# Optimization experiments

Measured on AMD Instinct MI355X. Metric: run time of the kernel, lower is better.

The kernel has to match this reference:

```python
import jax, jax.numpy as jnp
import numpy as np

N = 2048   # total nodes (16 graphs x 128 EEG channels)
BS = 16    # number of graphs
E = 65536  # directed edges
LENIN = 8500
H = 640


def _lstm_layer(x, w_ih, w_hh, b_ih, b_hh):
    # x: [T, in]; torch gate order i, f, g, o. Input projection hoisted out of scan.
    hdim = w_hh.shape[1]
    xp = x @ w_ih.T + (b_ih + b_hh)  # [T, 4H]
    def step(carry, xt):
        h, c = carry
        g = xt + h @ w_hh.T
        i, f, gg, o = jnp.split(g, 4)
        c = jax.nn.sigmoid(f) * c + jax.nn.sigmoid(i) * jnp.tanh(gg)
        h = jax.nn.sigmoid(o) * jnp.tanh(c)
        return (h, c), h
    init = (jnp.zeros((hdim,), x.dtype), jnp.zeros((hdim,), x.dtype))
    _, hs = jax.lax.scan(step, init, xp)
    return hs  # [T, H]


def _gcn(x, W, b, src, dst, n):
    # PyG GCNConv: add self-loops, symmetric deg^-1/2 normalization, scatter-add at target.
    xw = x @ W
    loop = jnp.arange(n)
    s = jnp.concatenate([src, loop])
    d = jnp.concatenate([dst, loop])
    deg = jax.ops.segment_sum(jnp.ones(d.shape[0], xw.dtype), d, num_segments=n)
    dinv = jnp.where(deg > 0, jax.lax.rsqrt(jnp.maximum(deg, 1e-12)), 0.0)
    norm = dinv[s] * dinv[d]
    out = jax.ops.segment_sum(xw[s] * norm[:, None], d, num_segments=n)
    return out + b


def _bn(x):
    # F.batch_norm(training=True, no running stats, no affine): biased var, eps=1e-5
    mu = jnp.mean(x, axis=0)
    var = jnp.mean((x - mu) ** 2, axis=0)
    return (x - mu) * jax.lax.rsqrt(var + 1e-5)


def _lrelu(x):
    return jnp.where(x >= 0, x, 0.01 * x)


def setup_inputs() -> dict:
    key = jax.random.key(0)
    ks = jax.random.split(key, 32)
    s = 0.05
    inp = {}
    inp['x_in'] = jax.random.normal(ks[0], (N, LENIN), dtype=jnp.float32)
    inp['edge_index'] = jax.random.randint(ks[1], (2, E), 0, N).astype(jnp.int64)
    # LSTM: 3 layers
    ins = [LENIN, H, H]
    for l in range(3):
        inp[f'lstm_w_ih_{l}'] = s * jax.random.normal(ks[2 + 4 * l], (4 * H, ins[l]), dtype=jnp.float32)
        inp[f'lstm_w_hh_{l}'] = s * jax.random.normal(ks[3 + 4 * l], (4 * H, H), dtype=jnp.float32)
        inp[f'lstm_b_ih_{l}'] = s * jax.random.normal(ks[4 + 4 * l], (4 * H,), dtype=jnp.float32)
        inp[f'lstm_b_hh_{l}'] = s * jax.random.normal(ks[5 + 4 * l], (4 * H,), dtype=jnp.float32)
    # GCN layers
    dims = [(640, 320), (320, 180), (180, 90), (90, 50)]
    for i, (di, do) in enumerate(dims, 1):
        inp[f'gcn_w{i}'] = s * jax.random.normal(ks[14 + 2 * i], (di, do), dtype=jnp.float32)
        inp[f'gcn_b{i}'] = jnp.zeros((do,), dtype=jnp.float32)
    # FC head
    fdims = [(50, 32), (32, 16), (16, 1)]
    for i, (di, do) in enumerate(fdims, 1):
        inp[f'fc_w{i}'] = s * jax.random.normal(ks[24 + 2 * i], (di, do), dtype=jnp.float32)
        inp[f'fc_b{i}'] = jnp.zeros((do,), dtype=jnp.float32)
    return inp


def reference(x_in, edge_index,
              lstm_w_ih_0, lstm_w_hh_0, lstm_b_ih_0, lstm_b_hh_0,
              lstm_w_ih_1, lstm_w_hh_1, lstm_b_ih_1, lstm_b_hh_1,
              lstm_w_ih_2, lstm_w_hh_2, lstm_b_ih_2, lstm_b_hh_2,
              gcn_w1, gcn_b1, gcn_w2, gcn_b2, gcn_w3, gcn_b3, gcn_w4, gcn_b4,
              fc_w1, fc_b1, fc_w2, fc_b2, fc_w3, fc_b3):
    x = _lstm_layer(x_in, lstm_w_ih_0, lstm_w_hh_0, lstm_b_ih_0, lstm_b_hh_0)
    x = _lstm_layer(x, lstm_w_ih_1, lstm_w_hh_1, lstm_b_ih_1, lstm_b_hh_1)
    x = _lstm_layer(x, lstm_w_ih_2, lstm_w_hh_2, lstm_b_ih_2, lstm_b_hh_2)
    src, dst = edge_index[0], edge_index[1]
    x = _bn(_lrelu(_gcn(x, gcn_w1, gcn_b1, src, dst, N)))
    x = _bn(_lrelu(_gcn(x, gcn_w2, gcn_b2, src, dst, N)))
    x = _bn(_lrelu(_gcn(x, gcn_w3, gcn_b3, src, dst, N)))
    x = _bn(_lrelu(_gcn(x, gcn_w4, gcn_b4, src, dst, N)))
    # global_add_pool with batch = i // (N // BS): contiguous blocks -> reshape-sum
    emb = x.reshape(BS, N // BS, -1).sum(axis=1)  # [BS, 50]
    y = ((emb @ fc_w1 + fc_b1) @ fc_w2 + fc_b2) @ fc_w3 + fc_b3  # [BS, 1]
    return y, emb
```

## Files before the change

### kernel.cpp

```cpp
#include <hip/hip_runtime.h>
#include <stdint.h>

#define NNODES 2048
#define T_SEQ  2048
#define HD     640
#define GD     2560
#define KIN    8500
#define NEDGE  65536
#define NGRAPH 16
#define SB     64
#define SDP    10
#define REC64  256

typedef unsigned long long u64;
typedef _Float16 half2v __attribute__((ext_vector_type(2)));
using short8 = __attribute__((ext_vector_type(8))) short;
using f32x4  = __attribute__((ext_vector_type(4))) float;

#if __has_builtin(__builtin_amdgcn_fdot2)
#define HAVE_FDOT2 1
#endif

__device__ __forceinline__ float dot2acc(unsigned w, unsigned h, float acc) {
#ifdef HAVE_FDOT2
  return __builtin_amdgcn_fdot2(__builtin_bit_cast(half2v, w),
                                __builtin_bit_cast(half2v, h), acc, false);
#else
  acc += (float)__builtin_bit_cast(_Float16, (unsigned short)(w & 0xffffu)) *
         (float)__builtin_bit_cast(_Float16, (unsigned short)(h & 0xffffu));
  acc += (float)__builtin_bit_cast(_Float16, (unsigned short)(w >> 16)) *
         (float)__builtin_bit_cast(_Float16, (unsigned short)(h >> 16));
  return acc;
#endif
}

__device__ __forceinline__ unsigned short f2h(float x) {
  return __builtin_bit_cast(unsigned short, (_Float16)x);
}
__device__ __forceinline__ unsigned packh(float a, float b) {
  return (unsigned)f2h(a) | ((unsigned)f2h(b) << 16);
}
__device__ __forceinline__ unsigned f2bf(float x) {
  unsigned u = __float_as_uint(x);
  return (u + 0x7fffu + ((u >> 16) & 1u)) >> 16;
}
__device__ __forceinline__ unsigned packbf(float a, float b) {
  return f2bf(a) | (f2bf(b) << 16);
}

#define GK 32
__global__ __launch_bounds__(256) void gemm_mfma(
    const float* __restrict__ A, const float* __restrict__ W,
    const float* __restrict__ b1, const float* __restrict__ b2,
    float* __restrict__ C, int M, int N, int K) {
  __shared__ __align__(16) short As[128 * 40];
  __shared__ __align__(16) short Ws[128 * 40];
  const int tid = threadIdx.x;
  const int wave = tid >> 6, lane = tid & 63;
  const int bm = blockIdx.y * 128, bn = blockIdx.x * 128;
  const int wm = (wave >> 1) * 64, wn = (wave & 1) * 64;
  const int mrow = lane & 15, quad = lane >> 4;
  const int srow = tid >> 1, skc = (tid & 1) * 16;
  f32x4 acc[4][4] = {};
  for (int k0 = 0; k0 < K; k0 += GK) {
    float av[16], wv[16];
    if (k0 + GK <= K) {
      const float* Ap = A + (long)(bm + srow) * K + k0 + skc;
      const float* Wp = W + (long)(bn + srow) * K + k0 + skc;
#pragma unroll
      for (int i = 0; i < 4; i++) {
        float4 a4 = *(const float4*)(Ap + 4 * i);
        float4 w4 = *(const float4*)(Wp + 4 * i);
        av[4*i]=a4.x; av[4*i+1]=a4.y; av[4*i+2]=a4.z; av[4*i+3]=a4.w;
        wv[4*i]=w4.x; wv[4*i+1]=w4.y; wv[4*i+2]=w4.z; wv[4*i+3]=w4.w;
      }
    } else {
#pragma unroll
      for (int i = 0; i < 16; i++) {
        const int k = k0 + skc + i;
        av[i] = (k < K) ? A[(long)(bm + srow) * K + k] : 0.f;
        wv[i] = (k < K) ? W[(long)(bn + srow) * K + k] : 0.f;
      }
    }
    __syncthreads();
    {
      uint4* pa = (uint4*)&As[srow * 40 + skc];
      uint4* pw = (uint4*)&Ws[srow * 40 + skc];
      pa[0] = make_uint4(packbf(av[0],av[1]), packbf(av[2],av[3]),
                         packbf(av[4],av[5]), packbf(av[6],av[7]));
      pa[1] = make_uint4(packbf(av[8],av[9]), packbf(av[10],av[11]),
                         packbf(av[12],av[13]), packbf(av[14],av[15]));
      pw[0] = make_uint4(packbf(wv[0],wv[1]), packbf(wv[2],wv[3]),
                         packbf(wv[4],wv[5]), packbf(wv[6],wv[7]));
      pw[1] = make_uint4(packbf(wv[8],wv[9]), packbf(wv[10],wv[11]),
                         packbf(wv[12],wv[13]), packbf(wv[14],wv[15]));
    }
    __syncthreads();
    short8 af[4], bf[4];
#pragma unroll
    for (int mi = 0; mi < 4; mi++)
      af[mi] = *(const short8*)&As[(wm + mi * 16 + mrow) * 40 + quad * 8];
#pragma unroll
    for (int ni = 0; ni < 4; ni++)
      bf[ni] = *(const short8*)&Ws[(wn + ni * 16 + mrow) * 40 + quad * 8];
#pragma unroll
    for (int mi = 0; mi < 4; mi++)
#pragma unroll
      for (int ni = 0; ni < 4; ni++)
        acc[mi][ni] = __builtin_amdgcn_mfma_f32_16x16x32_bf16(
            af[mi], bf[ni], acc[mi][ni], 0, 0, 0);
  }
#pragma unroll
  for (int ni = 0; ni < 4; ni++) {
    const int c = bn + wn + ni * 16 + mrow;
    const float bias = b1[c] + b2[c];
#pragma unroll
    for (int mi = 0; mi < 4; mi++) {
      const int r0 = bm + wm + mi * 16 + quad * 4;
#pragma unroll
      for (int reg = 0; reg < 4; reg++)
        C[(long)(r0 + reg) * N + c] = acc[mi][ni][reg] + bias;
    }
  }
}

__global__ __launch_bounds__(256, 1) void fused_scan(
    const float* __restrict__ xp,
    const float* __restrict__ whh0,
    const float* __restrict__ wih1, const float* __restrict__ whh1,
    const float* __restrict__ bih1, const float* __restrict__ bhh1,
    const float* __restrict__ wih2, const float* __restrict__ whh2,
    const float* __restrict__ bih2, const float* __restrict__ bhh2,
    u64* __restrict__ rec0, u64* __restrict__ rec1, u64* __restrict__ rec2,
    float* __restrict__ hs2) {
  __shared__ uint4 wh[2 * 3200];
  __shared__ __align__(16) unsigned short hbufh[640];
  __shared__ __align__(16) unsigned short xbufh[640];
  __shared__ float pdot[2][4][40];
  const int tid = threadIdx.x;
  const int l = blockIdx.x / SB, b = blockIdx.x % SB;
  const int lane = tid & 63, wv = tid >> 6;

  const float* Wih = (l == 1) ? wih1 : wih2;
  const float* Whh = (l == 0) ? whh0 : ((l == 1) ? whh1 : whh2);
  const u64* recI = (l == 1) ? rec0 : rec1;
  u64* recO = (l == 0) ? rec0 : ((l == 1) ? rec1 : rec2);

  const int nstage = (l > 0) ? 6400 : 3200;
  for (int idx = tid; idx < nstage; idx += 256) {
    int rem = idx;
    const int mat = (rem < 3200) ? 1 : 0;
    if (mat == 0) rem -= 3200;
    const int r = rem / 80, kg = rem - r * 80;
    const int g = r / SDP, d = r - g * SDP;
    const long grow = (long)(g * HD + b * SDP + d) * HD;
    const float* wr = ((mat == 1) ? Whh : Wih) + grow + kg * 8;
    const float4 wa = *(const float4*)(wr);
    const float4 wb = *(const float4*)(wr + 4);
    wh[mat * 3200 + kg * 40 + r] =
        make_uint4(packh(wa.x, wa.y), packh(wa.z, wa.w),
                   packh(wb.x, wb.y), packh(wb.z, wb.w));
  }

  float ext = 0.f;
  int gxi = 0;
  if (wv == 0 && lane < 40) {
    const int g = lane / SDP, d = lane - g * SDP;
    gxi = g * HD + b * SDP + d;
    if (l == 0) {
      ext = xp[gxi];
    } else {
      const float* bi = (l == 1) ? bih1 : bih2;
      const float* bh = (l == 1) ? bhh1 : bhh2;
      ext = bi[gxi] + bh[gxi];
    }
  }
  __syncthreads();

  const int rid = wv * 16 + (lane >> 2), j = lane & 3;
  const int ubase = rid * SDP + 3 * j;
  unsigned short* hslot = hbufh + ubase;
  unsigned short* xslot = xbufh + ubase;

  float creg = 0.f;
  for (int t = 0; t < T_SEQ; t++) {
    unsigned pend = ((t > 0) ? 1u : 0u) | ((l > 0) ? 2u : 0u);
    const long io = (long)(t - 1) * REC64 + wv * 64 + lane;
    const long iu = (long)t * REC64 + wv * 64 + lane;
    long spins = 0;
    u64 vo = 0, vu = 0;
    while (__any(pend != 0)) {
      if (pend & 1u) vo = __hip_atomic_load(recO + io, __ATOMIC_RELAXED,
                                            __HIP_MEMORY_SCOPE_AGENT);
      if (pend & 2u) vu = __hip_atomic_load(recI + iu, __ATOMIC_RELAXED,
                                            __HIP_MEMORY_SCOPE_AGENT);
      if ((pend & 1u) && (unsigned)(vo >> 48) == (unsigned)t) {
        pend &= ~1u;
        const unsigned lo = (unsigned)vo, hi = (unsigned)(vo >> 32);
        hslot[0] = (unsigned short)lo;
        if (j < 3) { hslot[1] = (unsigned short)(lo >> 16);
                     hslot[2] = (unsigned short)hi; }
      }
      if ((pend & 2u) && (unsigned)(vu >> 48) == (unsigned)(t + 1)) {
        pend &= ~2u;
        const unsigned lo = (unsigned)vu, hi = (unsigned)(vu >> 32);
        xslot[0] = (unsigned short)lo;
        if (j < 3) { xslot[1] = (unsigned short)(lo >> 16);
                     xslot[2] = (unsigned short)hi; }
      }
      if (__any(pend != 0)) {
        if (++spins > 30000000L) break;
        __builtin_amdgcn_s_sleep(1);
      }
    }
    if (t == 0) {
      hslot[0] = 0;
      if (j < 3) { hslot[1] = 0; hslot[2] = 0; }
    }
    __threadfence_block();

    if (lane < 40) {
      const int kg0 = wv * 20;
      float acc0 = 0.f, acc1 = 0.f;
      const uint4* wp = &wh[3200 + kg0 * 40 + lane];
      const uint4* hb = ((const uint4*)hbufh) + kg0;
#pragma unroll
      for (int g = 0; g < 20; g += 2) {
        const uint4 wA = wp[g * 40];
        const uint4 hA = hb[g];
        acc0 = dot2acc(wA.x, hA.x, acc0); acc0 = dot2acc(wA.y, hA.y, acc0);
        acc0 = dot2acc(wA.z, hA.z, acc0); acc0 = dot2acc(wA.w, hA.w, acc0);
        const uint4 wB = wp[(g + 1) * 40];
        const uint4 hB = hb[g + 1];
        acc1 = dot2acc(wB.x, hB.x, acc1); acc1 = dot2acc(wB.y, hB.y, acc1);
        acc1 = dot2acc(wB.z, hB.z, acc1); acc1 = dot2acc(wB.w, hB.w, acc1);
      }
      if (l > 0) {
        const uint4* wq = &wh[kg0 * 40 + lane];
        const uint4* xb = ((const uint4*)xbufh) + kg0;
#pragma unroll
        for (int g = 0; g < 20; g += 2) {
          const uint4 wA = wq[g * 40];
          const uint4 xA = xb[g];
          acc0 = dot2acc(wA.x, xA.x, acc0); acc0 = dot2acc(wA.y, xA.y, acc0);
          acc0 = dot2acc(wA.z, xA.z, acc0); acc0 = dot2acc(wA.w, xA.w, acc0);
          const uint4 wB = wq[(g + 1) * 40];
          const uint4 xB = xb[g + 1];
          acc1 = dot2acc(wB.x, xB.x, acc1); acc1 = dot2acc(wB.y, xB.y, acc1);
          acc1 = dot2acc(wB.z, xB.z, acc1); acc1 = dot2acc(wB.w, xB.w, acc1);
        }
      }
      pdot[t & 1][wv][lane] = acc0 + acc1;
    }
    __syncthreads();

    if (wv == 0) {
      const int par = t & 1;
      float av = 0.f;
      if (lane < 40) {
        const float gsum = pdot[par][0][lane] + pdot[par][1][lane] +
                           pdot[par][2][lane] + pdot[par][3][lane] + ext;
        if (lane / SDP == 2) {
          const float e2 = __expf(2.f * gsum);
          av = 1.f - 2.f / (e2 + 1.f);
        } else {
          av = 1.f / (1.f + __expf(-gsum));
        }
      }
      const float ai = av;
      const float af = __shfl(av, lane + SDP);
      const float ag = __shfl(av, lane + 2 * SDP);
      const float ao = __shfl(av, lane + 3 * SDP);
      float h = 0.f;
      if (lane < SDP) {
        creg = af * creg + ai * ag;
        const float e2 = __expf(2.f * creg);
        h = ao * (1.f - 2.f / (e2 + 1.f));
        if (l == 2) hs2[(long)t * HD + b * SDP + lane] = h;
      }
      if (l == 0 && lane < 40 && t + 1 < T_SEQ)
        ext = xp[(long)(t + 1) * GD + gxi];
      const float ha = __shfl(h, 3 * lane);
      const float hb2 = __shfl(h, 3 * lane + 1);
      const float hc = __shfl(h, 3 * lane + 2);
      if (lane < 4) {
        const unsigned seq = (unsigned)(t + 1);
        const unsigned sa = f2h(ha);
        const unsigned sb = (lane < 3) ? f2h(hb2) : 0u;
        const unsigned sc = (lane < 3) ? f2h(hc) : 0u;
        const u64 val = (u64)(sa | (sb << 16)) | ((u64)(sc | (seq << 16)) << 32);
        __hip_atomic_store(recO + (long)t * REC64 + b * 4 + lane, val,
                           __ATOMIC_RELAXED, __HIP_MEMORY_SCOPE_AGENT);
      }
    }
  }
}

__global__ __launch_bounds__(256) void gcn_gemm(
    const float* __restrict__ X, const float* __restrict__ W,
    float* __restrict__ Y, int di, int dout) {
  __shared__ float xr[640];
  const int n = blockIdx.x;
  for (int k = threadIdx.x; k < di; k += 256) xr[k] = X[(long)n * di + k];
  __syncthreads();
  for (int c = threadIdx.x; c < dout; c += 256) {
    float acc = 0.f;
    for (int k = 0; k < di; k++) acc = fmaf(xr[k], W[(long)k * dout + c], acc);
    Y[(long)n * dout + c] = acc;
  }
}

__global__ void deg_kernel(const int* __restrict__ dst, unsigned int* __restrict__ deg) {
  const int e = blockIdx.x * 256 + threadIdx.x;
  if (e < NEDGE) atomicAdd(&deg[dst[e]], 1u);
}

__global__ void dinv_kernel(const unsigned int* __restrict__ deg, float* __restrict__ dinv) {
  const int n = blockIdx.x * 256 + threadIdx.x;
  if (n < NNODES) dinv[n] = 1.f / sqrtf((float)(deg[n] + 1u));
}

__global__ __launch_bounds__(128) void gcn_scatter(
    const float* __restrict__ XW, const int* __restrict__ src,
    const int* __restrict__ dst, const float* __restrict__ dinv,
    float* __restrict__ out, int dout) {
  const int e = blockIdx.x;
  const int s = src[e], d = dst[e];
  const float nrm = dinv[s] * dinv[d];
  for (int c = threadIdx.x; c < dout; c += 128)
    atomicAdd(&out[(long)d * dout + c], XW[(long)s * dout + c] * nrm);
}

__global__ __launch_bounds__(256) void gcn_bn(
    const float* __restrict__ scat, const float* __restrict__ xw,
    const float* __restrict__ dinv, const float* __restrict__ bias,
    float* __restrict__ out, int dout) {
  const int c = blockIdx.x;
  const float bc = bias[c];
  float s = 0.f, s2 = 0.f;
  for (int n = threadIdx.x; n < NNODES; n += 256) {
    float v = scat[(long)n * dout + c] + xw[(long)n * dout + c] * dinv[n] * dinv[n] + bc;
    v = v >= 0.f ? v : 0.01f * v;
    s += v; s2 += v * v;
  }
  __shared__ float rs[4], rs2[4];
#pragma unroll
  for (int off = 32; off; off >>= 1) { s += __shfl_down(s, off, 64); s2 += __shfl_down(s2, off, 64); }
  const int w = threadIdx.x >> 6;
  if ((threadIdx.x & 63) == 0) { rs[w] = s; rs2[w] = s2; }
  __syncthreads();
  const float ts  = rs[0] + rs[1] + rs[2] + rs[3];
  const float ts2 = rs2[0] + rs2[1] + rs2[2] + rs2[3];
  const float mu = ts * (1.f / (float)NNODES);
  const float var = ts2 * (1.f / (float)NNODES) - mu * mu;
  const float rstd = 1.f / sqrtf(var + 1e-5f);
  for (int n = threadIdx.x; n < NNODES; n += 256) {
    float v = scat[(long)n * dout + c] + xw[(long)n * dout + c] * dinv[n] * dinv[n] + bc;
    v = v >= 0.f ? v : 0.01f * v;
    out[(long)n * dout + c] = (v - mu) * rstd;
  }
}

__global__ __launch_bounds__(64) void pool_kernel(
    const float* __restrict__ x, float* __restrict__ emb, float* __restrict__ dout) {
  const int g = blockIdx.x, c = threadIdx.x;
  if (c >= 50) return;
  float s = 0.f;
  for (int r = 0; r < 128; r++) s += x[(long)(g * 128 + r) * 50 + c];
  emb[g * 50 + c] = s;
  dout[16 + g * 50 + c] = s;
}

__global__ __launch_bounds__(64) void fc_head(
    const float* __restrict__ emb,
    const float* __restrict__ w1, const float* __restrict__ b1,
    const float* __restrict__ w2, const float* __restrict__ b2,
    const float* __restrict__ w3, const float* __restrict__ b3,
    float* __restrict__ dout) {
  const int g = threadIdx.x;
  if (g >= NGRAPH) return;
  float e[50];
#pragma unroll
  for (int k = 0; k < 50; k++) e[k] = emb[g * 50 + k];
  float t1[32];
  for (int j = 0; j < 32; j++) {
    float a = b1[j];
    for (int k = 0; k < 50; k++) a = fmaf(e[k], w1[k * 32 + j], a);
    t1[j] = a;
  }
  float t2[16];
  for (int j = 0; j < 16; j++) {
    float a = b2[j];
    for (int k = 0; k < 32; k++) a = fmaf(t1[k], w2[k * 16 + j], a);
    t2[j] = a;
  }
  float y = b3[0];
  for (int k = 0; k < 16; k++) y = fmaf(t2[k], w3[k], y);
  dout[g] = y;
}

extern "C" void kernel_launch(void* const* d_in, const int* in_sizes, int n_in,
                              void* d_out, int out_size, void* d_ws, size_t ws_size,
                              hipStream_t stream) {
  const float* x_in  = (const float*)d_in[0];
  const int*   eidx  = (const int*)d_in[1];
  const float* w_ih[3] = {(const float*)d_in[2], (const float*)d_in[6],  (const float*)d_in[10]};
  const float* w_hh[3] = {(const float*)d_in[3], (const float*)d_in[7],  (const float*)d_in[11]};
  const float* b_ih[3] = {(const float*)d_in[4], (const float*)d_in[8],  (const float*)d_in[12]};
  const float* b_hh[3] = {(const float*)d_in[5], (const float*)d_in[9],  (const float*)d_in[13]};
  const float* gw[4] = {(const float*)d_in[14], (const float*)d_in[16], (const float*)d_in[18], (const float*)d_in[20]};
  const float* gbv[4] = {(const float*)d_in[15], (const float*)d_in[17], (const float*)d_in[19], (const float*)d_in[21]};
  const float* fw1 = (const float*)d_in[22]; const float* fb1 = (const float*)d_in[23];
  const float* fw2 = (const float*)d_in[24]; const float* fb2 = (const float*)d_in[25];
  const float* fw3 = (const float*)d_in[26]; const float* fb3 = (const float*)d_in[27];
  const int* src = eidx;
  const int* dst = eidx + NEDGE;

  float* ws  = (float*)d_ws;
  float* xp  = ws;
  u64* rec0 = (u64*)(ws + 5242880);
  u64* rec1 = rec0 + 524288;
  u64* rec2 = rec1 + 524288;
  float* hs2 = ws + 5242880 + 3145728;
  unsigned int* deg = (unsigned int*)(hs2 + 1310720);
  float* dinv = (float*)(deg + 2048);
  float* emb  = dinv + 2048;
  float* ga = xp;
  float* gb = xp + 655360;
  float* x0 = xp + 1310720;
  float* x1 = xp + 1966080;

  hipMemsetAsync(rec0, 0, (size_t)3 * 524288 * sizeof(u64), stream);
  hipMemsetAsync(deg, 0, 2048 * sizeof(unsigned int), stream);

  gemm_mfma<<<dim3(GD / 128, NNODES / 128), 256, 0, stream>>>(
      x_in, w_ih[0], b_ih[0], b_hh[0], xp, NNODES, GD, KIN);

  deg_kernel<<<NEDGE / 256, 256, 0, stream>>>(dst, deg);
  dinv_kernel<<<NNODES / 256, 256, 0, stream>>>(deg, dinv);

  fused_scan<<<3 * SB, 256, 0, stream>>>(
      xp, w_hh[0], w_ih[1], w_hh[1], b_ih[1], b_hh[1],
      w_ih[2], w_hh[2], b_ih[2], b_hh[2], rec0, rec1, rec2, hs2);

  const int dims_in[4]  = {640, 320, 180, 90};
  const int dims_out[4] = {320, 180, 90, 50};
  const float* xin_l[4] = {hs2, x0, x1, x0};
  float* xout_l[4]      = {x0, x1, x0, x1};
  for (int l = 0; l < 4; l++) {
    gcn_gemm<<<NNODES, 256, 0, stream>>>(xin_l[l], gw[l], ga, dims_in[l], dims_out[l]);
    hipMemsetAsync(gb, 0, (size_t)NNODES * dims_out[l] * sizeof(float), stream);
    gcn_scatter<<<NEDGE, 128, 0, stream>>>(ga, src, dst, dinv, gb, dims_out[l]);
    gcn_bn<<<dims_out[l], 256, 0, stream>>>(gb, ga, dinv, gbv[l], xout_l[l], dims_out[l]);
  }

  pool_kernel<<<NGRAPH, 64, 0, stream>>>(x1, emb, (float*)d_out);
  fc_head<<<1, 64, 0, stream>>>(emb, fw1, fb1, fw2, fb2, fw3, fb3, (float*)d_out);
}
```

Baseline: 6.700 ms.

## Repartition fused LSTM scan: 80 blocks per layer, weights held in registers

The persistent three-layer LSTM scan kernel is restructured from 64 blocks of 256 threads per layer (10 hidden dims each) to 80 blocks of 512 threads (8 dims each). Recurrent and input weights now live in per-thread registers instead of LDS, and each thread reduces a 40-element slice with a cross-half shuffle. Polling of the inter-block handoff records becomes per-lane with a short spin before sleeping, and the record row layout changes to 240 entries. The aim is shorter per-timestep critical-path latency through more parallelism and no LDS weight reads, at the cost of more blocks that must all be co-resident and more global spinning traffic.

```diff
diff --git a/kernel.cpp b/kernel.cpp
--- a/kernel.cpp
+++ b/kernel.cpp
@@ -8,9 +8,11 @@
 #define KIN    8500
 #define NEDGE  65536
 #define NGRAPH 16
-#define SB     64
-#define SDP    10
-#define REC64  256
+
+#define LSB    80
+#define LDIM   8
+#define ROW64  240
+#define RECL   (T_SEQ * ROW64)
 
 typedef unsigned long long u64;
 typedef _Float16 half2v __attribute__((ext_vector_type(2)));
@@ -124,7 +126,7 @@
   }
 }
 
-__global__ __launch_bounds__(256, 1) void fused_scan(
+__global__ __launch_bounds__(512, 2) void fused_scan(
     const float* __restrict__ xp,
     const float* __restrict__ whh0,
     const float* __restrict__ wih1, const float* __restrict__ whh1,
@@ -133,165 +135,143 @@
     const float* __restrict__ bih2, const float* __restrict__ bhh2,
     u64* __restrict__ rec0, u64* __restrict__ rec1, u64* __restrict__ rec2,
     float* __restrict__ hs2) {
-  __shared__ uint4 wh[2 * 3200];
+  const int l = blockIdx.x / LSB, blk = blockIdx.x % LSB;
+  const int tid = threadIdx.x, wv = tid >> 6, lane = tid & 63;
+
   __shared__ __align__(16) unsigned short hbufh[640];
   __shared__ __align__(16) unsigned short xbufh[640];
-  __shared__ float pdot[2][4][40];
-  const int tid = threadIdx.x;
-  const int l = blockIdx.x / SB, b = blockIdx.x % SB;
-  const int lane = tid & 63, wv = tid >> 6;
+  __shared__ float pdot[2][8][32];
 
   const float* Wih = (l == 1) ? wih1 : wih2;
   const float* Whh = (l == 0) ? whh0 : ((l == 1) ? whh1 : whh2);
-  const u64* recI = (l == 1) ? rec0 : rec1;
-  u64* recO = (l == 0) ? rec0 : ((l == 1) ? rec1 : rec2);
-
-  const int nstage = (l > 0) ? 6400 : 3200;
-  for (int idx = tid; idx < nstage; idx += 256) {
-    int rem = idx;
-    const int mat = (rem < 3200) ? 1 : 0;
-    if (mat == 0) rem -= 3200;
-    const int r = rem / 80, kg = rem - r * 80;
-    const int g = r / SDP, d = r - g * SDP;
-    const long grow = (long)(g * HD + b * SDP + d) * HD;
-    const float* wr = ((mat == 1) ? Whh : Wih) + grow + kg * 8;
-    const float4 wa = *(const float4*)(wr);
-    const float4 wb = *(const float4*)(wr + 4);
-    wh[mat * 3200 + kg * 40 + r] =
-        make_uint4(packh(wa.x, wa.y), packh(wa.z, wa.w),
-                   packh(wb.x, wb.y), packh(wb.z, wb.w));
-  }
-
-  float ext = 0.f;
-  int gxi = 0;
-  if (wv == 0 && lane < 40) {
-    const int g = lane / SDP, d = lane - g * SDP;
-    gxi = g * HD + b * SDP + d;
-    if (l == 0) {
-      ext = xp[gxi];
-    } else {
-      const float* bi = (l == 1) ? bih1 : bih2;
-      const float* bh = (l == 1) ? bhh1 : bhh2;
-      ext = bi[gxi] + bh[gxi];
-    }
-  }
+  const float* bi  = (l == 1) ? bih1 : bih2;
+  const float* bh  = (l == 1) ? bhh1 : bhh2;
+  u64* recL = (l == 0) ? rec0 : ((l == 1) ? rec1 : rec2);
+  const u64* recU = (l == 1) ? rec0 : rec1;
+
+  const int r = lane & 31, kh = lane >> 5;
+  const int gq = r >> 3, dd = r & 7;
+  const long wro = (long)(gq * HD + blk * LDIM + dd) * HD + 80 * wv + 40 * kh;
+  unsigned wh[20], wx[20];
+#pragma unroll
+  for (int i = 0; i < 10; ++i) {
+    float4 a = *(const float4*)(Whh + wro + 4 * i);
+    wh[2 * i]     = packh(a.x, a.y);
+    wh[2 * i + 1] = packh(a.z, a.w);
+  }
+  if (l > 0) {
+#pragma unroll
+    for (int i = 0; i < 10; ++i) {
+      float4 a = *(const float4*)(Wih + wro + 4 * i);
+      wx[2 * i]     = packh(a.x, a.y);
+      wx[2 * i + 1] = packh(a.z, a.w);
+    }
+  }
+
+  const int gidx = (lane >> 3) * HD + blk * LDIM + (lane & 7);
+  float extb = 0.f, creg = 0.f;
+  if (wv == 0 && lane < 32)
+    extb = (l == 0) ? xp[gidx] : (bi[gidx] + bh[gidx]);
+
+  unsigned* hbuf32 = (unsigned*)hbufh;
+  unsigned* xbuf32 = (unsigned*)xbufh;
+  if (lane < 40) { hbuf32[40 * wv + lane] = 0; xbuf32[40 * wv + lane] = 0; }
   __syncthreads();
 
-  const int rid = wv * 16 + (lane >> 2), j = lane & 3;
-  const int ubase = rid * SDP + 3 * j;
-  unsigned short* hslot = hbufh + ubase;
-  unsigned short* xslot = xbufh + ubase;
-
-  float creg = 0.f;
-  for (int t = 0; t < T_SEQ; t++) {
-    unsigned pend = ((t > 0) ? 1u : 0u) | ((l > 0) ? 2u : 0u);
-    const long io = (long)(t - 1) * REC64 + wv * 64 + lane;
-    const long iu = (long)t * REC64 + wv * 64 + lane;
-    long spins = 0;
-    u64 vo = 0, vu = 0;
-    while (__any(pend != 0)) {
-      if (pend & 1u) vo = __hip_atomic_load(recO + io, __ATOMIC_RELAXED,
-                                            __HIP_MEMORY_SCOPE_AGENT);
-      if (pend & 2u) vu = __hip_atomic_load(recI + iu, __ATOMIC_RELAXED,
-                                            __HIP_MEMORY_SCOPE_AGENT);
-      if ((pend & 1u) && (unsigned)(vo >> 48) == (unsigned)t) {
-        pend &= ~1u;
-        const unsigned lo = (unsigned)vo, hi = (unsigned)(vo >> 32);
-        hslot[0] = (unsigned short)lo;
-        if (j < 3) { hslot[1] = (unsigned short)(lo >> 16);
-                     hslot[2] = (unsigned short)hi; }
-      }
-      if ((pend & 2u) && (unsigned)(vu >> 48) == (unsigned)(t + 1)) {
-        pend &= ~2u;
-        const unsigned lo = (unsigned)vu, hi = (unsigned)(vu >> 32);
-        xslot[0] = (unsigned short)lo;
-        if (j < 3) { xslot[1] = (unsigned short)(lo >> 16);
-                     xslot[2] = (unsigned short)hi; }
-      }
-      if (__any(pend != 0)) {
-        if (++spins > 30000000L) break;
-        __builtin_amdgcn_s_sleep(1);
-      }
-    }
-    if (t == 0) {
-      hslot[0] = 0;
-      if (j < 3) { hslot[1] = 0; hslot[2] = 0; }
+  const bool isA = (lane < 30);
+  const bool isB = (l > 0) && (lane >= 32) && (lane < 62);
+  const int p = isA ? lane : (lane - 32);
+  const int dimb = 80 * wv + (p / 3) * LDIM + 3 * (p % 3);
+  const int ncnt = ((p % 3) == 2) ? 2 : 3;
+  unsigned short* slot = (isA ? hbufh : xbufh) + dimb;
+
+  long totspins = 0;
+  for (int t = 0; t < T_SEQ; ++t) {
+    const bool want = (isA && t > 0) || isB;
+    if (want && totspins < 30000000L) {
+      const u64* src = isA ? (recL + (long)(t - 1) * ROW64 + 30 * wv + p)
+                           : (recU + (long)t * ROW64 + 30 * wv + p);
+      const unsigned exps = isA ? (unsigned)t : (unsigned)(t + 1);
+      int ss = 0;
+      for (;;) {
+        const u64 v = __hip_atomic_load(src, __ATOMIC_RELAXED,
+                                        __HIP_MEMORY_SCOPE_AGENT);
+        if ((unsigned)(v >> 48) == exps) {
+          slot[0] = (unsigned short)v;
+          slot[1] = (unsigned short)(v >> 16);
+          if (ncnt == 3) slot[2] = (unsigned short)(v >> 32);
+          break;
+        }
+        ++totspins;
+        if (++ss > 2) __builtin_amdgcn_s_sleep(1);
+        if (totspins > 30000000L) break;
+      }
     }
     __threadfence_block();
 
-    if (lane < 40) {
-      const int kg0 = wv * 20;
-      float acc0 = 0.f, acc1 = 0.f;
-      const uint4* wp = &wh[3200 + kg0 * 40 + lane];
-      const uint4* hb = ((const uint4*)hbufh) + kg0;
-#pragma unroll
-      for (int g = 0; g < 20; g += 2) {
-        const uint4 wA = wp[g * 40];
-        const uint4 hA = hb[g];
-        acc0 = dot2acc(wA.x, hA.x, acc0); acc0 = dot2acc(wA.y, hA.y, acc0);
-        acc0 = dot2acc(wA.z, hA.z, acc0); acc0 = dot2acc(wA.w, hA.w, acc0);
-        const uint4 wB = wp[(g + 1) * 40];
-        const uint4 hB = hb[g + 1];
-        acc1 = dot2acc(wB.x, hB.x, acc1); acc1 = dot2acc(wB.y, hB.y, acc1);
-        acc1 = dot2acc(wB.z, hB.z, acc1); acc1 = dot2acc(wB.w, hB.w, acc1);
-      }
-      if (l > 0) {
-        const uint4* wq = &wh[kg0 * 40 + lane];
-        const uint4* xb = ((const uint4*)xbufh) + kg0;
-#pragma unroll
-        for (int g = 0; g < 20; g += 2) {
-          const uint4 wA = wq[g * 40];
-          const uint4 xA = xb[g];
-          acc0 = dot2acc(wA.x, xA.x, acc0); acc0 = dot2acc(wA.y, xA.y, acc0);
-          acc0 = dot2acc(wA.z, xA.z, acc0); acc0 = dot2acc(wA.w, xA.w, acc0);
-          const uint4 wB = wq[(g + 1) * 40];
-          const uint4 xB = xb[g + 1];
-          acc1 = dot2acc(wB.x, xB.x, acc1); acc1 = dot2acc(wB.y, xB.y, acc1);
-          acc1 = dot2acc(wB.z, xB.z, acc1); acc1 = dot2acc(wB.w, xB.w, acc1);
-        }
-      }
-      pdot[t & 1][wv][lane] = acc0 + acc1;
-    }
+    unsigned hc[20];
+    {
+      const uint4* hb = (const uint4*)&hbuf32[40 * wv + 20 * kh];
+#pragma unroll
+      for (int i = 0; i < 5; ++i) {
+        uint4 q = hb[i];
+        hc[4*i] = q.x; hc[4*i+1] = q.y; hc[4*i+2] = q.z; hc[4*i+3] = q.w;
+      }
+    }
+    float a = 0.f;
+#pragma unroll
+    for (int i = 0; i < 20; ++i) a = dot2acc(wh[i], hc[i], a);
+    if (l > 0) {
+      const uint4* xb = (const uint4*)&xbuf32[40 * wv + 20 * kh];
+#pragma unroll
+      for (int i = 0; i < 5; ++i) {
+        uint4 q = xb[i];
+        hc[4*i] = q.x; hc[4*i+1] = q.y; hc[4*i+2] = q.z; hc[4*i+3] = q.w;
+      }
+#pragma unroll
+      for (int i = 0; i < 20; ++i) a = dot2acc(wx[i], hc[i], a);
+    }
+    a += __shfl_xor(a, 32);
+    if (lane < 32) pdot[t & 1][wv][lane] = a;
     __syncthreads();
 
     if (wv == 0) {
       const int par = t & 1;
       float av = 0.f;
-      if (lane < 40) {
-        const float gsum = pdot[par][0][lane] + pdot[par][1][lane] +
-                           pdot[par][2][lane] + pdot[par][3][lane] + ext;
-        if (lane / SDP == 2) {
-          const float e2 = __expf(2.f * gsum);
+      if (lane < 32) {
+        float s = extb;
+#pragma unroll
+        for (int w = 0; w < 8; ++w) s += pdot[par][w][lane];
+        if ((lane >> 3) == 2) {
+          const float e2 = __expf(2.f * s);
           av = 1.f - 2.f / (e2 + 1.f);
         } else {
-          av = 1.f / (1.f + __expf(-gsum));
+          av = 1.f / (1.f + __expf(-s));
         }
       }
       const float ai = av;
-      const float af = __shfl(av, lane + SDP);
-      const float ag = __shfl(av, lane + 2 * SDP);
-      const float ao = __shfl(av, lane + 3 * SDP);
+      const float af = __shfl(av, lane + 8);
+      const float ag = __shfl(av, lane + 16);
+      const float ao = __shfl(av, lane + 24);
       float h = 0.f;
-      if (lane < SDP) {
+      if (lane < LDIM) {
         creg = af * creg + ai * ag;
         const float e2 = __expf(2.f * creg);
         h = ao * (1.f - 2.f / (e2 + 1.f));
-        if (l == 2) hs2[(long)t * HD + b * SDP + lane] = h;
-      }
-      if (l == 0 && lane < 40 && t + 1 < T_SEQ)
-        ext = xp[(long)(t + 1) * GD + gxi];
+        if (l == 2) hs2[(long)t * HD + blk * LDIM + lane] = h;
+      }
       const float ha = __shfl(h, 3 * lane);
       const float hb2 = __shfl(h, 3 * lane + 1);
-      const float hc = __shfl(h, 3 * lane + 2);
-      if (lane < 4) {
+      const float hc2 = __shfl(h, 3 * lane + 2);
+      if (lane < 3) {
         const unsigned seq = (unsigned)(t + 1);
-        const unsigned sa = f2h(ha);
-        const unsigned sb = (lane < 3) ? f2h(hb2) : 0u;
-        const unsigned sc = (lane < 3) ? f2h(hc) : 0u;
-        const u64 val = (u64)(sa | (sb << 16)) | ((u64)(sc | (seq << 16)) << 32);
-        __hip_atomic_store(recO + (long)t * REC64 + b * 4 + lane, val,
+        const u64 val = (u64)((unsigned)f2h(ha) | ((unsigned)f2h(hb2) << 16)) |
+                        ((u64)((unsigned)f2h(hc2) | (seq << 16)) << 32);
+        __hip_atomic_store(recL + (long)t * ROW64 + 3 * blk + lane, val,
                            __ATOMIC_RELAXED, __HIP_MEMORY_SCOPE_AGENT);
       }
+      if (l == 0 && lane < 32 && t + 1 < T_SEQ)
+        extb = xp[(long)(t + 1) * GD + gidx];
     }
   }
 }
@@ -419,9 +399,9 @@
   float* ws  = (float*)d_ws;
   float* xp  = ws;
   u64* rec0 = (u64*)(ws + 5242880);
-  u64* rec1 = rec0 + 524288;
-  u64* rec2 = rec1 + 524288;
-  float* hs2 = ws + 5242880 + 3145728;
+  u64* rec1 = rec0 + RECL;
+  u64* rec2 = rec1 + RECL;
+  float* hs2 = ws + 5242880 + 2949120;
   unsigned int* deg = (unsigned int*)(hs2 + 1310720);
   float* dinv = (float*)(deg + 2048);
   float* emb  = dinv + 2048;
@@ -430,7 +410,7 @@
   float* x0 = xp + 1310720;
   float* x1 = xp + 1966080;
 
-  hipMemsetAsync(rec0, 0, (size_t)3 * 524288 * sizeof(u64), stream);
+  hipMemsetAsync(rec0, 0, (size_t)3 * RECL * sizeof(u64), stream);
   hipMemsetAsync(deg, 0, 2048 * sizeof(unsigned int), stream);
 
   gemm_mfma<<<dim3(GD / 128, NNODES / 128), 256, 0, stream>>>(
@@ -439,7 +419,7 @@
   deg_kernel<<<NEDGE / 256, 256, 0, stream>>>(dst, deg);
   dinv_kernel<<<NNODES / 256, 256, 0, stream>>>(deg, dinv);
 
-  fused_scan<<<3 * SB, 256, 0, stream>>>(
+  fused_scan<<<3 * LSB, 512, 0, stream>>>(
       xp, w_hh[0], w_ih[1], w_hh[1], b_ih[1], b_hh[1],
       w_ih[2], w_hh[2], b_ih[2], b_hh[2], rec0, rec1, rec2, hs2);
 
```

Result: faster. 6.134 ms (-8.4%).
